# Kernel optimization log

Hardware: AMD Instinct MI355X
Metric: run time of the kernel (lower is better)

## Reference

```python
import jax, jax.numpy as jnp
import numpy as np

B, S = 64, 64
IMG_F, EMB, HID, VOCAB = 2048, 512, 512, 32000


def setup_inputs() -> dict:
    key = jax.random.key(0)
    ks = jax.random.split(key, 12)
    s = 0.02
    return {
        "img": jax.random.normal(ks[0], (B, IMG_F), jnp.float32),
        "captions": jax.random.randint(ks[1], (B, S), 0, VOCAB),
        "embed_W": jax.random.normal(ks[2], (VOCAB, EMB), jnp.float32) * s,
        "Wi": jax.random.normal(ks[3], (IMG_F, HID), jnp.float32) * s,
        "bi": jax.random.normal(ks[4], (HID,), jnp.float32) * s,
        "Wx": jax.random.normal(ks[5], (EMB, HID), jnp.float32) * s,
        "bx": jax.random.normal(ks[6], (HID,), jnp.float32) * s,
        "Wh": jax.random.normal(ks[7], (HID, HID), jnp.float32) * s,
        "bh": jax.random.normal(ks[8], (HID, HID)[:1] + (HID,), jnp.float32)[0] * s if False else jax.random.normal(ks[8], (HID,), jnp.float32) * s,
        "Wy": jax.random.normal(ks[9], (HID, VOCAB), jnp.float32) * s,
        "by": jax.random.normal(ks[10], (VOCAB,), jnp.float32) * s,
    }


def reference(img, captions, embed_W, Wi, bi, Wx, bx, Wh, bh, Wy, by):
    # Embed caption inputs (drop last token): (B, T, EMB), T = S-1
    x = embed_W[captions[:, :-1]]
    # Precompute input-to-hidden preactivations for all steps: (B, T, HID)
    pre = jnp.einsum("bte,eh->bth", x, Wx) + bx
    # Image features are injected only at t=0 (as in the torch loop)
    pre = pre.at[:, 0].add(img @ Wi + bi)

    def step(h_prev, p_t):
        h_t = jnp.tanh(p_t + h_prev @ Wh + bh)
        return h_t, h_t

    h0 = jnp.zeros((img.shape[0], Wh.shape[0]), dtype=x.dtype)
    _, hs = jax.lax.scan(step, h0, pre.transpose(1, 0, 2))  # (T, B, HID)
    hs = hs.transpose(1, 0, 2)  # (B, T, HID)
    # Output projection in one big GEMM (same math as per-step h2y)
    logits = jnp.einsum("bth,hv->btv", hs, Wy) + by  # (B, T, VOCAB)
    return logits
```

## Files before the change

### kernel.cpp

```cpp
#include <hip/hip_runtime.h>
#include <hip/hip_bf16.h>

#define B_    64
#define S_    64
#define T_    63
#define IMGF  2048
#define EMB   512
#define HID   512
#define VOCAB 32000
#define MROWS 4032
#define MPAD  4096
#define NTILES 2000

typedef __bf16 bf16;
typedef __bf16 bf16x8 __attribute__((ext_vector_type(8)));
typedef float  f32x4  __attribute__((ext_vector_type(4)));

__device__ __forceinline__ void gload_lds16(const void* g, void* l) {
  __builtin_amdgcn_global_load_lds(
      (const __attribute__((address_space(1))) unsigned int*)g,
      (__attribute__((address_space(3))) unsigned int*)l, 16, 0, 0);
}

#define LGKM_BARRIER() asm volatile("s_waitcnt lgkmcnt(0)\n\ts_barrier" ::: "memory")

__global__ __launch_bounds__(256) void transpose_w(
    const float* __restrict__ W, bf16* __restrict__ WT, int K, int N)
{
  __shared__ float tile[64][65];
  const int tx = threadIdx.x & 63, ty = threadIdx.x >> 6;
  const int n0 = blockIdx.x * 64, k0 = blockIdx.y * 64;
  #pragma unroll
  for (int r = ty; r < 64; r += 4)
    tile[r][tx] = W[(size_t)(k0 + r) * N + n0 + tx];
  __syncthreads();
  #pragma unroll
  for (int r = ty; r < 64; r += 4)
    WT[(size_t)(n0 + r) * K + k0 + tx] = (bf16)tile[tx][r];
}

__global__ __launch_bounds__(256) void transpose_wy_tiled(
    const float* __restrict__ W, bf16* __restrict__ T)
{
  __shared__ float tile[64][65];
  const int tx = threadIdx.x & 63, ty = threadIdx.x >> 6;
  const int n0 = blockIdx.x * 64, k0 = blockIdx.y * 64;
  #pragma unroll
  for (int r = ty; r < 64; r += 4)
    tile[r][tx] = W[(size_t)(k0 + r) * VOCAB + n0 + tx];
  __syncthreads();
  #pragma unroll
  for (int r = ty; r < 64; r += 4) {
    const int n = n0 + r, k = k0 + tx;
    const int bn = n >> 8, rr = n & 255, kt = k >> 5;
    const int sl = ((k & 31) >> 3) ^ ((rr >> 1) & 3);
    const size_t dst = (((size_t)(bn * 16 + kt) * 1024 + rr * 4 + sl) << 3)
                     + (k & 7);
    T[dst] = (bf16)tile[tx][r];
  }
}

__global__ __launch_bounds__(256) void embed_gather(
    const float* __restrict__ embW, const int* __restrict__ captions,
    bf16* __restrict__ X)
{
  const int r = blockIdx.x;
  const int tid = threadIdx.x;
  if (r < MROWS) {
    const int b = r / T_, t = r % T_;
    const int idx = captions[b * S_ + t];
    float2 v = ((const float2*)(embW + (size_t)idx * EMB))[tid];
    X[(size_t)r * EMB + 2 * tid]     = (bf16)v.x;
    X[(size_t)r * EMB + 2 * tid + 1] = (bf16)v.y;
  } else {
    X[(size_t)r * EMB + 2 * tid]     = (bf16)0.f;
    X[(size_t)r * EMB + 2 * tid + 1] = (bf16)0.f;
  }
}

__global__ __launch_bounds__(256) void img_to_bf16(
    const float* __restrict__ img, bf16* __restrict__ imgB)
{
  const int r = blockIdx.x;
  const int tid = threadIdx.x;
  #pragma unroll
  for (int j = 0; j < 8; j++) {
    const int c = tid + j * 256;
    const float v = (r < B_) ? img[(size_t)r * IMGF + c] : 0.f;
    imgB[(size_t)r * IMGF + c] = (bf16)v;
  }
}

__global__ __launch_bounds__(256) void gemm_bt(
    const bf16* __restrict__ A, const bf16* __restrict__ BT,
    const float* __restrict__ bias, float* __restrict__ C,
    int Mvalid, int N, int K)
{
  __shared__ __align__(16) bf16 As[2][128 * 32];
  __shared__ __align__(16) bf16 Bs[2][128 * 32];
  const int tid  = threadIdx.x;
  const int wave = tid >> 6, lane = tid & 63;
  const int wm = wave >> 1, wn = wave & 1;
  const int bm = blockIdx.x, bn = blockIdx.y;
  const int lg = lane >> 4, lr = lane & 15;

  f32x4 acc[4][4];
  #pragma unroll
  for (int m = 0; m < 4; m++)
    #pragma unroll
    for (int n = 0; n < 4; n++) acc[m][n] = (f32x4){0.f, 0.f, 0.f, 0.f};

  const bf16* Abase = A  + (size_t)bm * 128 * K;
  const bf16* Bbase = BT + (size_t)bn * 128 * K;

  const int c0 = wave * 64 + lane;
  const int r0 = c0 >> 2,  sl0 = (c0 & 3) ^ ((r0 >> 1) & 3);
  const int c1 = 256 + c0;
  const int r1 = c1 >> 2,  sl1 = (c1 & 3) ^ ((r1 >> 1) & 3);

  const int NT = K >> 5;

#define STAGE_TILE(buf, kt)                                                   \
  do {                                                                        \
    gload_lds16(Abase + (size_t)r0 * K + (kt) + sl0 * 8,                      \
                &As[buf][(wave * 64) * 8]);                                   \
    gload_lds16(Abase + (size_t)r1 * K + (kt) + sl1 * 8,                      \
                &As[buf][(256 + wave * 64) * 8]);                             \
    gload_lds16(Bbase + (size_t)r0 * K + (kt) + sl0 * 8,                      \
                &Bs[buf][(wave * 64) * 8]);                                   \
    gload_lds16(Bbase + (size_t)r1 * K + (kt) + sl1 * 8,                      \
                &Bs[buf][(256 + wave * 64) * 8]);                             \
  } while (0)

  STAGE_TILE(0, 0);
  int cur = 0;
  for (int it = 0; it < NT; ++it) {
    __syncthreads();
    if (it + 1 < NT) STAGE_TILE(cur ^ 1, (it + 1) * 32);

    bf16x8 af[4], bfr[4];
    #pragma unroll
    for (int m = 0; m < 4; m++) {
      const int r = wm * 64 + m * 16 + lr;
      const int sp = lg ^ ((r >> 1) & 3);
      af[m] = *(const bf16x8*)&As[cur][r * 32 + sp * 8];
    }
    #pragma unroll
    for (int n = 0; n < 4; n++) {
      const int r = wn * 64 + n * 16 + lr;
      const int sp = lg ^ ((r >> 1) & 3);
      bfr[n] = *(const bf16x8*)&Bs[cur][r * 32 + sp * 8];
    }
    #pragma unroll
    for (int m = 0; m < 4; m++)
      #pragma unroll
      for (int n = 0; n < 4; n++)
        acc[m][n] = __builtin_amdgcn_mfma_f32_16x16x32_bf16(af[m], bfr[n], acc[m][n], 0, 0, 0);
    cur ^= 1;
  }
#undef STAGE_TILE

  const int row0 = bm * 128 + wm * 64 + (lane >> 4) * 4;
  const int col0 = bn * 128 + wn * 64 + lr;
  #pragma unroll
  for (int m = 0; m < 4; m++) {
    #pragma unroll
    for (int n = 0; n < 4; n++) {
      const int col = col0 + n * 16;
      const float bv = bias[col];
      #pragma unroll
      for (int q = 0; q < 4; q++) {
        const int row = row0 + m * 16 + q;
        if (row < Mvalid) C[(size_t)row * N + col] = acc[m][n][q] + bv;
      }
    }
  }
}

#define FREG 48
#define FLDS 16
__global__ __launch_bounds__(512, 1) void rnn_gemm(
    const float* __restrict__ pre, const bf16* __restrict__ WhT,
    const float* __restrict__ bh, const float* __restrict__ pimg,
    bf16* __restrict__ hs, const bf16* __restrict__ Btile,
    const float* __restrict__ by, float* __restrict__ C,
    unsigned* ctrl)
{
  __shared__ __align__(16) char smem[147456];
  const int tid  = threadIdx.x;
  const int wave = tid >> 6, lane = tid & 63;
  const int lg = lane >> 4, lr = lane & 15;

  if (blockIdx.x < 4) {
    const int bg  = blockIdx.x;
    const int gb0 = bg * 16;
    const int wc0 = wave * 64;
    bf16* hsh = (bf16*)smem;
    bf16* bls = (bf16*)(smem + 16384);

    bf16x8 bw[FREG];
    #pragma unroll
    for (int f = 0; f < 64; f++) {
      const int n = f >> 4, kf = f & 15;
      const bf16x8 v = *(const bf16x8*)(WhT + (size_t)(wc0 + n * 16 + lr) * 512
                                            + kf * 32 + lg * 8);
      if (f < FREG) bw[f] = v;
      else *(bf16x8*)&bls[((wave * FLDS + (f - FREG)) * 64 + lane) * 8] = v;
    }

    *(f32x4*)&hsh[tid * 16]     = (f32x4){0.f, 0.f, 0.f, 0.f};
    *(f32x4*)&hsh[tid * 16 + 8] = (f32x4){0.f, 0.f, 0.f, 0.f};

    float bhv[4];
    #pragma unroll
    for (int n = 0; n < 4; n++) bhv[n] = bh[wc0 + n * 16 + lr];
    const float* preb = pre + ((size_t)(gb0 + lg * 4) * T_) * 512 + wc0 + lr;

    __syncthreads();

    #pragma unroll 1
    for (int t = 0; t < T_; t++) {
      float prq[4][4];
      #pragma unroll
      for (int n = 0; n < 4; n++)
        #pragma unroll
        for (int q = 0; q < 4; q++)
          prq[n][q] = preb[(size_t)q * (T_ * 512) + (size_t)t * 512 + n * 16];

      f32x4 acc[4];
      #pragma unroll
      for (int n = 0; n < 4; n++) acc[n] = (f32x4){0.f, 0.f, 0.f, 0.f};

      #pragma unroll
      for (int kf = 0; kf < 16; kf++) {
        const int c = (kf * 4 + lg) ^ (lr & 7);
        const bf16x8 a = *(const bf16x8*)&hsh[(lr * 64 + c) * 8];
        #pragma unroll
        for (int n = 0; n < 4; n++) {
          const int f = n * 16 + kf;
          bf16x8 bfrag;
          if (f < FREG) bfrag = bw[f];
          else bfrag = *(const bf16x8*)&bls[((wave * FLDS + (f - FREG)) * 64 + lane) * 8];
          acc[n] = __builtin_amdgcn_mfma_f32_16x16x32_bf16(a, bfrag, acc[n], 0, 0, 0);
        }
      }
      LGKM_BARRIER();

      #pragma unroll
      for (int n = 0; n < 4; n++) {
        #pragma unroll
        for (int q = 0; q < 4; q++) {
          const int bl = lg * 4 + q;
          const int b  = gb0 + bl;
          const int k  = wc0 + n * 16 + lr;
          float s = acc[n][q] + prq[n][q] + bhv[n];
          if (t == 0) s += pimg[(size_t)b * HID + k];
          const float e = __builtin_exp2f(s * 2.885390081777927f);
          const float hv = 1.f - 2.f * __builtin_amdgcn_rcpf(e + 1.f);
          hs[((size_t)t * 64 + b) * HID + k] = (bf16)hv;
          const int c = (k >> 3) ^ (bl & 7);
          hsh[bl * 512 + c * 8 + (k & 7)] = (bf16)hv;
        }
      }
      __syncthreads();
      if (tid == 0)
        __hip_atomic_store(&ctrl[bg], (unsigned)(t + 1),
                           __ATOMIC_RELEASE, __HIP_MEMORY_SCOPE_AGENT);
    }
    __syncthreads();
  }

  bf16* base = (bf16*)smem;
#define SMBUF(buf, op) (base + ((buf) * 2 + (op)) * 8192)
  unsigned* idsl = (unsigned*)(smem + 131072);

  const int wm = wave >> 2, wn = wave & 3;

  const int ca0 = tid,        ra0 = ca0 >> 2, sa0 = (ca0 & 3) ^ ((ra0 >> 1) & 3);
  const int ca1 = tid + 512,  ra1 = ca1 >> 2, sa1 = (ca1 & 3) ^ ((ra1 >> 1) & 3);
  const int ldsb0 = (wave * 64) * 8;
  const int ldsb1 = (512 + wave * 64) * 8;

  for (;;) {
    if (tid == 0) *idsl = atomicAdd(&ctrl[8], 1u);
    __syncthreads();
    const unsigned id = *idsl;
    if (id >= (unsigned)NTILES) break;
    const int bm = (int)(id / 125u), bn = (int)(id % 125u);

    if (tid == 0) {
      const unsigned tneed = (bm == 15) ? 63u : (unsigned)(4 * bm + 4);
      #pragma unroll
      for (int g = 0; g < 4; ++g) {
        int poll = 0;
        while (__hip_atomic_load(&ctrl[g], __ATOMIC_RELAXED,
                                 __HIP_MEMORY_SCOPE_AGENT) < tneed) {
          __builtin_amdgcn_s_sleep(8);
          if ((++poll & 63) == 0)
            (void)__hip_atomic_load(&ctrl[g], __ATOMIC_ACQUIRE,
                                    __HIP_MEMORY_SCOPE_AGENT);
        }
      }
    }
    __syncthreads();
    __builtin_amdgcn_fence(__ATOMIC_ACQUIRE, "agent");

    const bf16* Abase = hs + (size_t)bm * 256 * 512;

    f32x4 acc[8][4];
    #pragma unroll
    for (int m = 0; m < 8; m++)
      #pragma unroll
      for (int n = 0; n < 4; n++) acc[m][n] = (f32x4){0.f, 0.f, 0.f, 0.f};

#define STAGE256(buf, kti)                                                    \
  do {                                                                        \
    const bf16* Bt_ = Btile + (((size_t)bn * 16 + (kti)) << 13);              \
    gload_lds16(Abase + (size_t)ra0 * 512 + (kti) * 32 + sa0 * 8,             \
                SMBUF(buf, 0) + ldsb0);                                       \
    gload_lds16(Abase + (size_t)ra1 * 512 + (kti) * 32 + sa1 * 8,             \
                SMBUF(buf, 0) + ldsb1);                                       \
    gload_lds16(Bt_ + (size_t)tid * 8,         SMBUF(buf, 1) + ldsb0);        \
    gload_lds16(Bt_ + (size_t)(tid + 512) * 8, SMBUF(buf, 1) + ldsb1);        \
  } while (0)

    STAGE256(0, 0);
    STAGE256(1, 1);
    STAGE256(2, 2);

    #pragma unroll 1
    for (int it = 0; it < 16; ++it) {
      const int newer = (15 - it) > 2 ? 2 : (15 - it);
      switch (newer) {
        case 2:  asm volatile("s_waitcnt vmcnt(8)\n\ts_barrier" ::: "memory"); break;
        case 1:  asm volatile("s_waitcnt vmcnt(4)\n\ts_barrier" ::: "memory"); break;
        default: asm volatile("s_waitcnt vmcnt(0)\n\ts_barrier" ::: "memory"); break;
      }

      const bf16* As_ = SMBUF(it & 3, 0);
      const bf16* Bs_ = SMBUF(it & 3, 1);
      bf16x8 af[8], bfr[4];
      #pragma unroll
      for (int m = 0; m < 8; m++) {
        const int r = wm * 128 + m * 16 + lr;
        const int sp = lg ^ ((r >> 1) & 3);
        af[m] = *(const bf16x8*)&As_[(r * 4 + sp) * 8];
      }
      #pragma unroll
      for (int n = 0; n < 4; n++) {
        const int r = wn * 64 + n * 16 + lr;
        const int sp = lg ^ ((r >> 1) & 3);
        bfr[n] = *(const bf16x8*)&Bs_[(r * 4 + sp) * 8];
      }
      #pragma unroll
      for (int m = 0; m < 8; m++)
        #pragma unroll
        for (int n = 0; n < 4; n++)
          acc[m][n] = __builtin_amdgcn_mfma_f32_16x16x32_bf16(af[m], bfr[n], acc[m][n], 0, 0, 0);

      LGKM_BARRIER();
      if (it + 3 < 16) STAGE256((it + 3) & 3, it + 3);
    }
#undef STAGE256

    float* cst = (float*)smem;
    float bvv[4];
    #pragma unroll
    for (int n = 0; n < 4; n++)
      bvv[n] = by[bn * 256 + wn * 64 + n * 16 + lr];

    #pragma unroll
    for (int pass = 0; pass < 2; ++pass) {
      if (wm == pass) {
        #pragma unroll
        for (int m = 0; m < 8; m++)
          #pragma unroll
          for (int n = 0; n < 4; n++) {
            const int cc = wn * 64 + n * 16 + lr;
            #pragma unroll
            for (int q = 0; q < 4; q++)
              cst[(m * 16 + lg * 4 + q) * 256 + cc] = acc[m][n][q] + bvv[n];
          }
      }
      __syncthreads();
      const int rbase = bm * 256 + pass * 128;
      #pragma unroll
      for (int i = 0; i < 16; i++) {
        const int r = i * 8 + wave;
        const int grow = rbase + r;
        const int tt = grow >> 6, bb = grow & 63;
        if (tt < T_) {
          const f32x4 v = *(const f32x4*)&cst[r * 256 + lane * 4];
          *(f32x4*)&C[(size_t)(bb * T_ + tt) * VOCAB + bn * 256 + lane * 4] = v;
        }
      }
      __syncthreads();
    }
  }
#undef SMBUF
}

extern "C" void kernel_launch(void* const* d_in, const int* in_sizes, int n_in,
                              void* d_out, int out_size, void* d_ws, size_t ws_size,
                              hipStream_t stream) {
  const float* img      = (const float*)d_in[0];
  const int*   captions = (const int*)d_in[1];
  const float* embW     = (const float*)d_in[2];
  const float* Wi       = (const float*)d_in[3];
  const float* bi       = (const float*)d_in[4];
  const float* Wx       = (const float*)d_in[5];
  const float* bx       = (const float*)d_in[6];
  const float* Wh       = (const float*)d_in[7];
  const float* bh       = (const float*)d_in[8];
  const float* Wy       = (const float*)d_in[9];
  const float* by       = (const float*)d_in[10];
  float* logits = (float*)d_out;

  char* ws = (char*)d_ws;
  bf16*  WyT  = (bf16*)(ws);
  bf16*  WxT  = (bf16*)(ws + 32768000);
  bf16*  X    = (bf16*)(ws + 33292288);
  bf16*  hs   = (bf16*)(ws + 37486592);
  float* pre  = (float*)(ws + 41680896);
  float* pimg = (float*)(ws + 49938432);
  unsigned* ctrl = (unsigned*)(ws + 50069504);
  bf16*  imgB = (bf16*)(ws + 50200576);
  bf16*  WiT  = (bf16*)(ws + 50724864);
  bf16*  WhT  = WxT;

  transpose_wy_tiled<<<dim3(VOCAB / 64, HID / 64), 256, 0, stream>>>(Wy, WyT);
  transpose_w<<<dim3(HID / 64, EMB / 64), 256, 0, stream>>>(Wx, WxT, EMB, HID);
  transpose_w<<<dim3(HID / 64, IMGF / 64), 256, 0, stream>>>(Wi, WiT, IMGF, HID);
  img_to_bf16<<<128, 256, 0, stream>>>(img, imgB);

  embed_gather<<<MPAD, 256, 0, stream>>>(embW, captions, X);

  gemm_bt<<<dim3(MPAD / 128, HID / 128), 256, 0, stream>>>(X, WxT, bx, pre, MROWS, HID, HID);

  gemm_bt<<<dim3(1, HID / 128), 256, 0, stream>>>(imgB, WiT, bi, pimg, B_, HID, IMGF);

  transpose_w<<<dim3(HID / 64, HID / 64), 256, 0, stream>>>(Wh, WhT, HID, HID);

  hipMemsetAsync(hs + (size_t)MROWS * HID, 0,
                 (size_t)(MPAD - MROWS) * HID * sizeof(bf16), stream);
  hipMemsetAsync(ctrl, 0, 256, stream);

  rnn_gemm<<<256, 512, 0, stream>>>(pre, WhT, bh, pimg, hs, WyT, by, logits, ctrl);
}
```

Measured before the change: 707.5 us.

## Assign fixed vocab-column tiles per block and signal recurrence progress every four steps

The output GEMM changes from a dynamic atomic tile queue of 256x256 tiles to a static assignment: each of 250 blocks owns one 256-column vocab strip and half of each 256-row M block, looping over the 16 M blocks in order. The Wy layout and LDS tiles move to K=64 chunks with a double buffer and an 8-way XOR swizzle. The recurrence blocks publish progress only every 4 steps, using a lighter LDS barrier otherwise. This aims to cut queue atomics and synchronisation overhead and keep each block's B strip cache-resident, at the cost of load-balancing flexibility and a fixed grid-size assumption.

```diff
diff --git a/kernel.cpp b/kernel.cpp
--- a/kernel.cpp
+++ b/kernel.cpp
@@ -10,7 +10,6 @@
 #define VOCAB 32000
 #define MROWS 4032
 #define MPAD  4096
-#define NTILES 2000
 
 typedef __bf16 bf16;
 typedef __bf16 bf16x8 __attribute__((ext_vector_type(8)));
@@ -52,9 +51,10 @@
   #pragma unroll
   for (int r = ty; r < 64; r += 4) {
     const int n = n0 + r, k = k0 + tx;
-    const int bn = n >> 8, rr = n & 255, kt = k >> 5;
-    const int sl = ((k & 31) >> 3) ^ ((rr >> 1) & 3);
-    const size_t dst = (((size_t)(bn * 16 + kt) * 1024 + rr * 4 + sl) << 3)
+    const int bn = n >> 8, rr = n & 255;
+    const int kt = k >> 6;
+    const int sl = ((k & 63) >> 3) ^ (rr & 7);
+    const size_t dst = (((size_t)(bn * 8 + kt) * 2048 + rr * 8 + sl) << 3)
                      + (k & 7);
     T[dst] = (bf16)tile[tx][r];
   }
@@ -262,34 +262,39 @@
           hsh[bl * 512 + c * 8 + (k & 7)] = (bf16)hv;
         }
       }
-      __syncthreads();
-      if (tid == 0)
-        __hip_atomic_store(&ctrl[bg], (unsigned)(t + 1),
-                           __ATOMIC_RELEASE, __HIP_MEMORY_SCOPE_AGENT);
-    }
-    __syncthreads();
-  }
-
-  bf16* base = (bf16*)smem;
-#define SMBUF(buf, op) (base + ((buf) * 2 + (op)) * 8192)
-  unsigned* idsl = (unsigned*)(smem + 131072);
-
+      if (((t + 1) & 3) == 0 || (t + 1) == T_) {
+        __syncthreads();
+        if (tid == 0)
+          __hip_atomic_store(&ctrl[bg], (unsigned)(t + 1),
+                             __ATOMIC_RELEASE, __HIP_MEMORY_SCOPE_AGENT);
+      } else {
+        LGKM_BARRIER();
+      }
+    }
+    return;
+  }
+
+  const int u = (int)blockIdx.x - 4;
+  if (u >= 250) return;
+  const int bn = u >> 1, half = u & 1;
+
+  bf16* smA = (bf16*)smem;
+  bf16* smB = (bf16*)(smem + 32768);
   const int wm = wave >> 2, wn = wave & 3;
 
-  const int ca0 = tid,        ra0 = ca0 >> 2, sa0 = (ca0 & 3) ^ ((ra0 >> 1) & 3);
-  const int ca1 = tid + 512,  ra1 = ca1 >> 2, sa1 = (ca1 & 3) ^ ((ra1 >> 1) & 3);
-  const int ldsb0 = (wave * 64) * 8;
-  const int ldsb1 = (512 + wave * 64) * 8;
-
-  for (;;) {
-    if (tid == 0) *idsl = atomicAdd(&ctrl[8], 1u);
-    __syncthreads();
-    const unsigned id = *idsl;
-    if (id >= (unsigned)NTILES) break;
-    const int bm = (int)(id / 125u), bn = (int)(id % 125u);
-
+  int raA[2], saA[2];
+  #pragma unroll
+  for (int i = 0; i < 2; i++) {
+    const int c = tid + i * 512;
+    raA[i] = c >> 3;
+    saA[i] = (c & 7) ^ (raA[i] & 7);
+  }
+
+  #pragma unroll 1
+  for (int bm = 0; bm < 16; ++bm) {
     if (tid == 0) {
-      const unsigned tneed = (bm == 15) ? 63u : (unsigned)(4 * bm + 4);
+      unsigned tneed = (unsigned)(4 * bm + 4);
+      if (tneed > 63u) tneed = 63u;
       #pragma unroll
       for (int g = 0; g < 4; ++g) {
         int poll = 0;
@@ -305,63 +310,63 @@
     __syncthreads();
     __builtin_amdgcn_fence(__ATOMIC_ACQUIRE, "agent");
 
-    const bf16* Abase = hs + (size_t)bm * 256 * 512;
-
-    f32x4 acc[8][4];
-    #pragma unroll
-    for (int m = 0; m < 8; m++)
+    const bf16* Ab = hs + ((size_t)bm * 256 + half * 128) * 512;
+
+    f32x4 acc[4][4];
+    #pragma unroll
+    for (int m = 0; m < 4; m++)
       #pragma unroll
       for (int n = 0; n < 4; n++) acc[m][n] = (f32x4){0.f, 0.f, 0.f, 0.f};
 
-#define STAGE256(buf, kti)                                                    \
+#define STAGEF(buf, kti)                                                      \
   do {                                                                        \
-    const bf16* Bt_ = Btile + (((size_t)bn * 16 + (kti)) << 13);              \
-    gload_lds16(Abase + (size_t)ra0 * 512 + (kti) * 32 + sa0 * 8,             \
-                SMBUF(buf, 0) + ldsb0);                                       \
-    gload_lds16(Abase + (size_t)ra1 * 512 + (kti) * 32 + sa1 * 8,             \
-                SMBUF(buf, 0) + ldsb1);                                       \
-    gload_lds16(Bt_ + (size_t)tid * 8,         SMBUF(buf, 1) + ldsb0);        \
-    gload_lds16(Bt_ + (size_t)(tid + 512) * 8, SMBUF(buf, 1) + ldsb1);        \
+    const bf16* Bt_ = Btile + (((size_t)(bn * 8 + (kti))) << 14);             \
+    _Pragma("unroll")                                                         \
+    for (int i = 0; i < 2; i++)                                               \
+      gload_lds16(Ab + (size_t)raA[i] * 512 + (kti) * 64 + saA[i] * 8,        \
+                  &smA[((buf) * 1024 + i * 512 + wave * 64) * 8]);            \
+    _Pragma("unroll")                                                         \
+    for (int i = 0; i < 4; i++)                                               \
+      gload_lds16(Bt_ + (size_t)(tid + i * 512) * 8,                          \
+                  &smB[((buf) * 2048 + i * 512 + wave * 64) * 8]);            \
   } while (0)
 
-    STAGE256(0, 0);
-    STAGE256(1, 1);
-    STAGE256(2, 2);
+    STAGEF(0, 0);
+    STAGEF(1, 1);
 
     #pragma unroll 1
-    for (int it = 0; it < 16; ++it) {
-      const int newer = (15 - it) > 2 ? 2 : (15 - it);
-      switch (newer) {
-        case 2:  asm volatile("s_waitcnt vmcnt(8)\n\ts_barrier" ::: "memory"); break;
-        case 1:  asm volatile("s_waitcnt vmcnt(4)\n\ts_barrier" ::: "memory"); break;
-        default: asm volatile("s_waitcnt vmcnt(0)\n\ts_barrier" ::: "memory"); break;
-      }
-
-      const bf16* As_ = SMBUF(it & 3, 0);
-      const bf16* Bs_ = SMBUF(it & 3, 1);
-      bf16x8 af[8], bfr[4];
-      #pragma unroll
-      for (int m = 0; m < 8; m++) {
-        const int r = wm * 128 + m * 16 + lr;
-        const int sp = lg ^ ((r >> 1) & 3);
-        af[m] = *(const bf16x8*)&As_[(r * 4 + sp) * 8];
-      }
-      #pragma unroll
-      for (int n = 0; n < 4; n++) {
-        const int r = wn * 64 + n * 16 + lr;
-        const int sp = lg ^ ((r >> 1) & 3);
-        bfr[n] = *(const bf16x8*)&Bs_[(r * 4 + sp) * 8];
-      }
-      #pragma unroll
-      for (int m = 0; m < 8; m++)
-        #pragma unroll
-        for (int n = 0; n < 4; n++)
-          acc[m][n] = __builtin_amdgcn_mfma_f32_16x16x32_bf16(af[m], bfr[n], acc[m][n], 0, 0, 0);
+    for (int it = 0; it < 8; ++it) {
+      if (it < 7) asm volatile("s_waitcnt vmcnt(6)\n\ts_barrier" ::: "memory");
+      else        asm volatile("s_waitcnt vmcnt(0)\n\ts_barrier" ::: "memory");
+
+      const bf16* As_ = smA + (it & 1) * 1024 * 8;
+      const bf16* Bs_ = smB + (it & 1) * 2048 * 8;
+      #pragma unroll
+      for (int kk = 0; kk < 2; kk++) {
+        bf16x8 af[4], bfr[4];
+        #pragma unroll
+        for (int m = 0; m < 4; m++) {
+          const int r = wm * 64 + m * 16 + lr;
+          const int sp = (kk * 4 + lg) ^ (r & 7);
+          af[m] = *(const bf16x8*)&As_[(r * 8 + sp) * 8];
+        }
+        #pragma unroll
+        for (int n = 0; n < 4; n++) {
+          const int r = wn * 64 + n * 16 + lr;
+          const int sp = (kk * 4 + lg) ^ (r & 7);
+          bfr[n] = *(const bf16x8*)&Bs_[(r * 8 + sp) * 8];
+        }
+        #pragma unroll
+        for (int m = 0; m < 4; m++)
+          #pragma unroll
+          for (int n = 0; n < 4; n++)
+            acc[m][n] = __builtin_amdgcn_mfma_f32_16x16x32_bf16(af[m], bfr[n], acc[m][n], 0, 0, 0);
+      }
 
       LGKM_BARRIER();
-      if (it + 3 < 16) STAGE256((it + 3) & 3, it + 3);
-    }
-#undef STAGE256
+      if (it + 2 < 8) STAGEF(it & 1, it + 2);
+    }
+#undef STAGEF
 
     float* cst = (float*)smem;
     float bvv[4];
@@ -373,7 +378,7 @@
     for (int pass = 0; pass < 2; ++pass) {
       if (wm == pass) {
         #pragma unroll
-        for (int m = 0; m < 8; m++)
+        for (int m = 0; m < 4; m++)
           #pragma unroll
           for (int n = 0; n < 4; n++) {
             const int cc = wn * 64 + n * 16 + lr;
@@ -383,9 +388,9 @@
           }
       }
       __syncthreads();
-      const int rbase = bm * 256 + pass * 128;
-      #pragma unroll
-      for (int i = 0; i < 16; i++) {
+      const int rbase = bm * 256 + half * 128 + pass * 64;
+      #pragma unroll
+      for (int i = 0; i < 8; i++) {
         const int r = i * 8 + wave;
         const int grow = rbase + r;
         const int tt = grow >> 6, bb = grow & 63;
@@ -397,7 +402,6 @@
       __syncthreads();
     }
   }
-#undef SMBUF
 }
 
 extern "C" void kernel_launch(void* const* d_in, const int* in_sizes, int n_in,
```

Measured after the change: 818.3 us. 1.16x slower.
